# Kernel optimization log

Hardware: AMD Instinct MI355X
Metric: run time of the kernel (lower is better)

## Reference

```python
import jax, jax.numpy as jnp
import numpy as np

BETA = 0.25  # commitment-loss weight from init_kwargs

B, T, D, K = 16, 2048, 256, 1024


def setup_inputs() -> dict:
    key = jax.random.key(0)
    k1, k2 = jax.random.split(key)
    z_e = jax.random.normal(k1, (B, T, D), dtype=jnp.float32)
    codebook = jax.random.normal(k2, (K, D), dtype=jnp.float32)
    return {"z_e": z_e, "codebook": codebook}


def reference(z_e, codebook):
    # dot_z_embedding: tensordot over channel dim -> (B, T, K)
    dot = jnp.einsum("btd,kd->btk", z_e, codebook)
    norm_sq_z = jnp.sum(jnp.square(z_e), axis=-1, keepdims=True)      # (B, T, 1)
    norm_sq_e = jnp.sum(jnp.square(codebook), axis=-1)                # (K,)
    dist = -2.0 * dot + norm_sq_z + norm_sq_e                         # (B, T, K)
    ids = jnp.argmin(dist, axis=-1)                                   # (B, T) int
    z_q = codebook[ids]                                               # (B, T, D)
    # losses: tf.norm over the quantised axis, then mean
    loss_commit = jnp.mean(jnp.linalg.norm(jax.lax.stop_gradient(z_e) - z_q, axis=-1))
    loss_codebook = jnp.mean(jnp.linalg.norm(z_e - jax.lax.stop_gradient(z_q), axis=-1))
    loss_vq = loss_codebook + BETA * loss_commit
    similarity = dot / jnp.sqrt(norm_sq_z) / jnp.sqrt(norm_sq_e)      # (B, T, K) cosine
    return z_q, similarity, ids, loss_vq
```

## Files before the change

kernel.cpp:

```cpp
#include <hip/hip_runtime.h>


#define M_ROWS 32768
#define KCODES 1024
#define DDIM   256
#define ENC_BIG 33554432.0f

typedef __bf16 bf16_t;
typedef __attribute__((ext_vector_type(8))) bf16_t bf16x8;
typedef __attribute__((ext_vector_type(4))) float f32x4;

__device__ __forceinline__ unsigned short f2bf(float f) {
  unsigned u = __float_as_uint(f);
  u += 0x7FFFu + ((u >> 16) & 1u);
  return (unsigned short)(u >> 16);
}

__device__ __forceinline__ float wave_sum(float p) {
#pragma unroll
  for (int o = 1; o < 64; o <<= 1) p += __shfl_xor(p, o);
  return p;
}
__device__ __forceinline__ float wave_min(float p) {
#pragma unroll
  for (int o = 1; o < 64; o <<= 1) p = fminf(p, __shfl_xor(p, o));
  return p;
}

__global__ __launch_bounds__(256) void prep_kernel(
    const float* __restrict__ ze, const float* __restrict__ cb,
    unsigned short* __restrict__ zb, unsigned short* __restrict__ cbb,
    float* __restrict__ rsqz,
    float* __restrict__ nse, float* __restrict__ rsqe)
{
  const int t = threadIdx.x;
  const int lane = t & 63;
  const int row = blockIdx.x * 4 + (t >> 6);
  if (row < M_ROWS) {
    const float4 z = ((const float4*)ze)[(size_t)row * 64 + lane];
    ushort4 u;
    u.x = f2bf(z.x); u.y = f2bf(z.y); u.z = f2bf(z.z); u.w = f2bf(z.w);
    ((ushort4*)zb)[(size_t)row * 64 + lane] = u;
    float p = wave_sum(z.x*z.x + z.y*z.y + z.z*z.z + z.w*z.w);
    if (lane == 0) rsqz[row] = 1.0f / sqrtf(p);
  } else {
    const int r = row - M_ROWS;
    const float4 e = ((const float4*)cb)[(size_t)r * 64 + lane];
    ushort4 u;
    u.x = f2bf(e.x); u.y = f2bf(e.y); u.z = f2bf(e.z); u.w = f2bf(e.w);
    ((ushort4*)cbb)[(size_t)r * 64 + lane] = u;
    float p = wave_sum(e.x*e.x + e.y*e.y + e.z*e.z + e.w*e.w);
    if (lane == 0) { nse[r] = p; rsqe[r] = 1.0f / sqrtf(p); }
  }
}

__global__ __launch_bounds__(256, 2) void gemm_kernel(
    const unsigned short* __restrict__ zb, const unsigned short* __restrict__ cbb,
    const float* __restrict__ rsqz, const float* __restrict__ rsqe_g,
    const float* __restrict__ nse_g,
    float* __restrict__ sim, float* __restrict__ cand)
{
  __shared__ __attribute__((aligned(128))) unsigned short lds[2][16384];
  const int tid  = threadIdx.x;
  const int wv   = tid >> 6, lane = tid & 63;
  const int bid  = blockIdx.x;
  const int swz  = (bid & 7) * 256 + (bid >> 3);
  const long row0 = (long)(swz >> 3) * 128;
  const int  col0 = (swz & 7) * 128;

  f32x4 acc[4][4] = {};

  const int rr = lane >> 3, qq = lane & 7;
  const int sq = ((qq ^ rr) << 3);

  auto stage = [&](int buf, int kt) {
    const int k0 = kt * 64;
#pragma unroll
    for (int i = 0; i < 4; ++i) {
      const int rbase = wv * 32 + i * 8;
      const unsigned short* srca = zb  + ((size_t)(row0 + rbase + rr)) * DDIM + k0 + sq;
      const unsigned short* srcb = cbb + ((size_t)(col0 + rbase + rr)) * DDIM + k0 + sq;
      __builtin_amdgcn_global_load_lds((const __attribute__((address_space(1))) void*)srca,
                                       (__attribute__((address_space(3))) void*)&lds[buf][rbase * 64],
                                       16, 0, 0);
      __builtin_amdgcn_global_load_lds((const __attribute__((address_space(1))) void*)srcb,
                                       (__attribute__((address_space(3))) void*)&lds[buf][8192 + rbase * 64],
                                       16, 0, 0);
    }
  };

  stage(0, 0);
  __syncthreads();

  const int r16 = lane & 15, g = lane >> 4;
#pragma unroll
  for (int kt = 0; kt < 4; ++kt) {
    if (kt < 3) stage((kt + 1) & 1, kt + 1);
    const unsigned short* cur = lds[kt & 1];
#pragma unroll
    for (int ks = 0; ks < 2; ++ks) {
      bf16x8 af[4], bfr[4];
#pragma unroll
      for (int mi = 0; mi < 4; ++mi) {
        const int r  = (wv >> 1) * 64 + mi * 16 + r16;
        const int qy = ((ks * 4 + g) ^ (r & 7)) << 4;
        af[mi] = *(const bf16x8*)((const char*)cur + r * 128 + qy);
      }
#pragma unroll
      for (int ni = 0; ni < 4; ++ni) {
        const int r  = (wv & 1) * 64 + ni * 16 + r16;
        const int qy = ((ks * 4 + g) ^ (r & 7)) << 4;
        bfr[ni] = *(const bf16x8*)((const char*)cur + 16384 + r * 128 + qy);
      }
#pragma unroll
      for (int mi = 0; mi < 4; ++mi)
#pragma unroll
        for (int ni = 0; ni < 4; ++ni)
          acc[mi][ni] = __builtin_amdgcn_mfma_f32_16x16x32_bf16(af[mi], bfr[ni], acc[mi][ni], 0, 0, 0);
    }
    __syncthreads();
  }

  const int wm = wv >> 1, wn = wv & 1;
  const int strip = (col0 >> 6) | wn;
#pragma unroll
  for (int mi = 0; mi < 4; ++mi) {
#pragma unroll
    for (int j = 0; j < 4; ++j) {
      const long row = row0 + wm * 64 + mi * 16 + g * 4 + j;
      const float rz = rsqz[row];
      float* so = sim + (size_t)row * KCODES + col0 + wn * 64 + r16;
      float e1 = ENC_BIG, e2 = ENC_BIG;
#pragma unroll
      for (int ni = 0; ni < 4; ++ni) {
        const int colk = col0 + wn * 64 + ni * 16 + r16;
        const float d = acc[mi][ni][j];
        so[ni * 16] = d * rz * rsqe_g[colk];
        const float v = nse_g[colk] - 2.0f * d;
        const float enc = floorf((v + 1024.0f) * 8.0f) * 1024.0f + (float)colk;
        if (enc < e1) { e2 = e1; e1 = enc; } else e2 = fminf(e2, enc);
      }
#pragma unroll
      for (int m = 1; m < 16; m <<= 1) {
        const float p1 = __shfl_xor(e1, m);
        const float p2 = __shfl_xor(e2, m);
        const float n1 = fminf(e1, p1);
        const float n2 = fminf(fmaxf(e1, p1), fminf(e2, p2));
        e1 = n1; e2 = n2;
      }
      if (r16 == 0)
        ((float2*)cand)[row * 16 + strip] = make_float2(e1, e2);
    }
  }
}

__global__ __launch_bounds__(256) void select1_kernel(
    const float* __restrict__ ze, const float* __restrict__ cb,
    const float* __restrict__ cand, const float* __restrict__ nse,
    const float* __restrict__ rsqz,
    float* __restrict__ ids, float* __restrict__ partials)
{
  __shared__ float s_part[4];
  const int t = threadIdx.x;
  const int lane = t & 63;
  const int row  = blockIdx.x * 4 + (t >> 6);

  const float e = (lane < 32) ? cand[(size_t)row * 32 + lane] : ENC_BIG;
  const float m_enc = wave_min(e);
  const float qmin  = floorf(m_enc * 0.0009765625f);
  const float ql    = floorf(e * 0.0009765625f);
  unsigned long long msk = __ballot(ql <= qmin + 16.0f);
  int kbest;
  float dmin;
  if (__popcll(msk) == 1) {
    kbest = ((int)m_enc) & 1023;
    dmin  = qmin * 0.125f - 1024.0f;
  } else {
    const float4 zr = ((const float4*)ze)[(size_t)row * 64 + lane];
    float tbest = INFINITY; kbest = KCODES;
    while (msk) {
      const int lb = __ffsll(msk) - 1;
      msk &= msk - 1;
      const int kc = ((int)__shfl(e, lb)) & 1023;
      const float4 er = ((const float4*)cb)[(size_t)kc * 64 + lane];
      const float p = wave_sum(zr.x*er.x + zr.y*er.y + zr.z*er.z + zr.w*er.w);
      const float tv = nse[kc] - 2.0f * p;
      if (tv < tbest || (tv == tbest && kc < kbest)) { tbest = tv; kbest = kc; }
    }
    dmin = tbest;
  }
  if (lane == 0) {
    const float rz = rsqz[row];
    const float nsz = 1.0f / (rz * rz);
    ids[row] = (float)kbest;
    s_part[t >> 6] = sqrtf(fmaxf(nsz + dmin, 0.0f));
  }
  __syncthreads();
  if (t == 0)
    partials[blockIdx.x] = (s_part[0] + s_part[1]) + (s_part[2] + s_part[3]);
}

__global__ __launch_bounds__(256) void zq_gather_kernel(
    const float* __restrict__ cb, const float* __restrict__ ids,
    float* __restrict__ zq)
{
  const int t = threadIdx.x;
  const int wv = t >> 6, lane = t & 63;
  const int row = blockIdx.x * 4 + wv;
  const int kbest = (int)ids[row];
  ((float4*)zq)[(size_t)row * 64 + lane] = ((const float4*)cb)[(size_t)kbest * 64 + lane];
}

__global__ __launch_bounds__(256) void finalize_kernel(
    const float* __restrict__ partials, float* __restrict__ out_loss)
{
  __shared__ float s[4];
  const int t = threadIdx.x;
  float p = 0.0f;
#pragma unroll
  for (int i = 0; i < 32; ++i) p += partials[t + i * 256];
  p = wave_sum(p);
  if ((t & 63) == 0) s[t >> 6] = p;
  __syncthreads();
  if (t == 0) out_loss[0] = 1.25f * ((s[0] + s[1]) + (s[2] + s[3])) / 32768.0f;
}

extern "C" void kernel_launch(void* const* d_in, const int* in_sizes, int n_in,
                              void* d_out, int out_size, void* d_ws, size_t ws_size,
                              hipStream_t stream) {
  const float* ze = (const float*)d_in[0];
  const float* cb = (const float*)d_in[1];

  float* out  = (float*)d_out;
  float* zq   = out;
  float* sim  = out + 8388608;
  float* ids  = out + 41943040;
  float* lout = out + 41975808;

  unsigned short* zb = (unsigned short*)d_out;
  float* cand = (float*)((char*)d_out + 16777216);

  char* w = (char*)d_ws;
  unsigned short* cbb = (unsigned short*)w;
  float* rsqz     = (float*)(w + 524288);
  float* nse      = (float*)(w + 655360);
  float* rsqe     = (float*)(w + 659456);
  float* partials = (float*)(w + 663552);

  prep_kernel<<<8448, 256, 0, stream>>>(ze, cb, zb, cbb, rsqz, nse, rsqe);
  gemm_kernel<<<2048, 256, 0, stream>>>(zb, cbb, rsqz, rsqe, nse, sim, cand);
  select1_kernel<<<8192, 256, 0, stream>>>(ze, cb, cand, nse, rsqz, ids, partials);
  zq_gather_kernel<<<8192, 256, 0, stream>>>(cb, ids, zq);
  finalize_kernel<<<1, 256, 0, stream>>>(partials, lout);
}
```

Baseline: 84.02 us.

## Keep 64-row A tile resident in LDS and stream all codebook columns per block

Each GEMM block now owns 64 rows of z, loads the full 64x256 A tile into LDS once, and loops over all 8 column tiles of the codebook, double-buffering B tiles and running the similarity/argmin epilogue after each column tile. The grid shrinks from 2048 to 512 blocks. This is meant to cut redundant reloads of z rows across column tiles and give fewer, longer-lived blocks. In exchange there are only 512 blocks (about two per CU), less MFMA work per wave per tile, and a serialized epilogue inside the loop, so latency hiding and occupancy may suffer.

```diff
diff --git a/kernel.cpp b/kernel.cpp
--- a/kernel.cpp
+++ b/kernel.cpp
@@ -60,96 +60,118 @@
     const float* __restrict__ nse_g,
     float* __restrict__ sim, float* __restrict__ cand)
 {
-  __shared__ __attribute__((aligned(128))) unsigned short lds[2][16384];
-  const int tid  = threadIdx.x;
-  const int wv   = tid >> 6, lane = tid & 63;
-  const int bid  = blockIdx.x;
-  const int swz  = (bid & 7) * 256 + (bid >> 3);
-  const long row0 = (long)(swz >> 3) * 128;
-  const int  col0 = (swz & 7) * 128;
-
-  f32x4 acc[4][4] = {};
+  __shared__ __attribute__((aligned(128))) unsigned short A[64 * 256];
+  __shared__ __attribute__((aligned(128))) unsigned short Bt[2][128 * 64];
+
+  const int t = threadIdx.x;
+  const int wv = t >> 6, lane = t & 63;
+  const long row0 = (long)blockIdx.x * 64;
+
+  const int r16 = lane & 15, g = lane >> 4;
+  const int wm = wv >> 1, wn = wv & 1;
+
+  {
+    const int p = lane & 31;
+#pragma unroll
+    for (int i = 0; i < 8; ++i) {
+      const int r = i * 8 + wv * 2 + (lane >> 5);
+      const int q = (p & 24) | ((p ^ (r & 7)) & 7);
+      const unsigned short* src = zb + (size_t)(row0 + r) * DDIM + q * 8;
+      __builtin_amdgcn_global_load_lds(
+          (const __attribute__((address_space(1))) void*)src,
+          (__attribute__((address_space(3))) void*)&A[(i * 8 + wv * 2) * 256],
+          16, 0, 0);
+    }
+  }
 
   const int rr = lane >> 3, qq = lane & 7;
   const int sq = ((qq ^ rr) << 3);
-
-  auto stage = [&](int buf, int kt) {
+  auto stageB = [&](int buf, int c, int kt) {
     const int k0 = kt * 64;
 #pragma unroll
     for (int i = 0; i < 4; ++i) {
       const int rbase = wv * 32 + i * 8;
-      const unsigned short* srca = zb  + ((size_t)(row0 + rbase + rr)) * DDIM + k0 + sq;
-      const unsigned short* srcb = cbb + ((size_t)(col0 + rbase + rr)) * DDIM + k0 + sq;
-      __builtin_amdgcn_global_load_lds((const __attribute__((address_space(1))) void*)srca,
-                                       (__attribute__((address_space(3))) void*)&lds[buf][rbase * 64],
-                                       16, 0, 0);
-      __builtin_amdgcn_global_load_lds((const __attribute__((address_space(1))) void*)srcb,
-                                       (__attribute__((address_space(3))) void*)&lds[buf][8192 + rbase * 64],
-                                       16, 0, 0);
+      const unsigned short* src = cbb + ((size_t)(c * 128 + rbase + rr)) * DDIM + k0 + sq;
+      __builtin_amdgcn_global_load_lds(
+          (const __attribute__((address_space(1))) void*)src,
+          (__attribute__((address_space(3))) void*)&Bt[buf][rbase * 64],
+          16, 0, 0);
     }
   };
 
-  stage(0, 0);
+  stageB(0, 0, 0);
   __syncthreads();
 
-  const int r16 = lane & 15, g = lane >> 4;
-#pragma unroll
-  for (int kt = 0; kt < 4; ++kt) {
-    if (kt < 3) stage((kt + 1) & 1, kt + 1);
-    const unsigned short* cur = lds[kt & 1];
+  f32x4 acc[2][4] = {};
+
+  for (int u = 0; u < 32; ++u) {
+    const int kt = u & 3;
+    if (u < 31) stageB((u + 1) & 1, (u + 1) >> 2, (u + 1) & 3);
+    const unsigned short* Bcur = Bt[u & 1];
+
 #pragma unroll
     for (int ks = 0; ks < 2; ++ks) {
-      bf16x8 af[4], bfr[4];
-#pragma unroll
-      for (int mi = 0; mi < 4; ++mi) {
-        const int r  = (wv >> 1) * 64 + mi * 16 + r16;
-        const int qy = ((ks * 4 + g) ^ (r & 7)) << 4;
-        af[mi] = *(const bf16x8*)((const char*)cur + r * 128 + qy);
+      const int q = kt * 8 + ks * 4 + g;
+      bf16x8 af[2], bfr[4];
+#pragma unroll
+      for (int mi = 0; mi < 2; ++mi) {
+        const int r  = wm * 32 + mi * 16 + r16;
+        const int ph = (q & 24) | ((q ^ (r & 7)) & 7);
+        af[mi] = *(const bf16x8*)((const char*)A + r * 512 + ph * 16);
       }
 #pragma unroll
       for (int ni = 0; ni < 4; ++ni) {
-        const int r  = (wv & 1) * 64 + ni * 16 + r16;
-        const int qy = ((ks * 4 + g) ^ (r & 7)) << 4;
-        bfr[ni] = *(const bf16x8*)((const char*)cur + 16384 + r * 128 + qy);
+        const int r  = wn * 64 + ni * 16 + r16;
+        const int ph = (ks * 4 + g) ^ (r & 7);
+        bfr[ni] = *(const bf16x8*)((const char*)Bcur + r * 128 + ph * 16);
       }
 #pragma unroll
-      for (int mi = 0; mi < 4; ++mi)
+      for (int mi = 0; mi < 2; ++mi)
 #pragma unroll
         for (int ni = 0; ni < 4; ++ni)
           acc[mi][ni] = __builtin_amdgcn_mfma_f32_16x16x32_bf16(af[mi], bfr[ni], acc[mi][ni], 0, 0, 0);
     }
     __syncthreads();
-  }
-
-  const int wm = wv >> 1, wn = wv & 1;
-  const int strip = (col0 >> 6) | wn;
-#pragma unroll
-  for (int mi = 0; mi < 4; ++mi) {
-#pragma unroll
-    for (int j = 0; j < 4; ++j) {
-      const long row = row0 + wm * 64 + mi * 16 + g * 4 + j;
-      const float rz = rsqz[row];
-      float* so = sim + (size_t)row * KCODES + col0 + wn * 64 + r16;
-      float e1 = ENC_BIG, e2 = ENC_BIG;
-#pragma unroll
-      for (int ni = 0; ni < 4; ++ni) {
-        const int colk = col0 + wn * 64 + ni * 16 + r16;
-        const float d = acc[mi][ni][j];
-        so[ni * 16] = d * rz * rsqe_g[colk];
-        const float v = nse_g[colk] - 2.0f * d;
-        const float enc = floorf((v + 1024.0f) * 8.0f) * 1024.0f + (float)colk;
-        if (enc < e1) { e2 = e1; e1 = enc; } else e2 = fminf(e2, enc);
+
+    if (kt == 3) {
+      const int c = u >> 2;
+      const int col0 = c * 128;
+      const int strip = c * 2 + wn;
+#pragma unroll
+      for (int mi = 0; mi < 2; ++mi) {
+#pragma unroll
+        for (int j = 0; j < 4; ++j) {
+          const int rloc = wm * 32 + mi * 16 + g * 4 + j;
+          const long row = row0 + rloc;
+          const float rz = rsqz[row];
+          float* so = sim + (size_t)row * KCODES + col0 + wn * 64 + r16;
+          float e1 = ENC_BIG, e2 = ENC_BIG;
+#pragma unroll
+          for (int ni = 0; ni < 4; ++ni) {
+            const int colk = col0 + wn * 64 + ni * 16 + r16;
+            const float d = acc[mi][ni][j];
+            so[ni * 16] = d * rz * rsqe_g[colk];
+            const float v = nse_g[colk] - 2.0f * d;
+            const float enc = floorf((v + 1024.0f) * 8.0f) * 1024.0f + (float)colk;
+            if (enc < e1) { e2 = e1; e1 = enc; } else e2 = fminf(e2, enc);
+          }
+#pragma unroll
+          for (int m = 1; m < 16; m <<= 1) {
+            const float p1 = __shfl_xor(e1, m);
+            const float p2 = __shfl_xor(e2, m);
+            const float n1 = fminf(e1, p1);
+            const float n2 = fminf(fmaxf(e1, p1), fminf(e2, p2));
+            e1 = n1; e2 = n2;
+          }
+          if (r16 == 0)
+            ((float2*)cand)[row * 16 + strip] = make_float2(e1, e2);
+        }
       }
 #pragma unroll
-      for (int m = 1; m < 16; m <<= 1) {
-        const float p1 = __shfl_xor(e1, m);
-        const float p2 = __shfl_xor(e2, m);
-        const float n1 = fminf(e1, p1);
-        const float n2 = fminf(fmaxf(e1, p1), fminf(e2, p2));
-        e1 = n1; e2 = n2;
-      }
-      if (r16 == 0)
-        ((float2*)cand)[row * 16 + strip] = make_float2(e1, e2);
+      for (int mi = 0; mi < 2; ++mi)
+#pragma unroll
+        for (int ni = 0; ni < 4; ++ni)
+          acc[mi][ni] = (f32x4)(0.0f);
     }
   }
 }
@@ -248,7 +270,7 @@
   float* partials = (float*)(w + 663552);
 
   prep_kernel<<<8448, 256, 0, stream>>>(ze, cb, zb, cbb, rsqz, nse, rsqe);
-  gemm_kernel<<<2048, 256, 0, stream>>>(zb, cbb, rsqz, rsqe, nse, sim, cand);
+  gemm_kernel<<<512, 256, 0, stream>>>(zb, cbb, rsqz, rsqe, nse, sim, cand);
   select1_kernel<<<8192, 256, 0, stream>>>(ze, cb, cand, nse, rsqz, ids, partials);
   zq_gather_kernel<<<8192, 256, 0, stream>>>(cb, ids, zq);
   finalize_kernel<<<1, 256, 0, stream>>>(partials, lout);
```

Result: slower. 90.88 us (+8.2%).
